# Kernel optimization log

Hardware: AMD Instinct MI355X
Metric: run time of the kernel (lower is better)

## Reference

```python
import jax, jax.numpy as jnp
import numpy as np

N_FEAT = 256
NUM_HEADS = 8
EPS = 1e-12  # torch F.normalize default eps


def setup_inputs() -> dict:
    key = jax.random.key(0)
    k1, k2, k3 = jax.random.split(key, 3)
    b, c, h, w = 1, N_FEAT, 64, 64
    x = jax.random.normal(k1, (b, c, h, w), dtype=jnp.float32)
    # 1x1 convs == channel GEMMs; store as (out_ch, in_ch) matrices
    w_qkv = jax.random.normal(k2, (3 * c, c), dtype=jnp.float32) * (1.0 / np.sqrt(c))
    w_proj = jax.random.normal(k3, (c, c), dtype=jnp.float32) * (1.0 / np.sqrt(c))
    temperature = jnp.ones((NUM_HEADS, 1, 1), dtype=jnp.float32)
    return {"x": x, "w_qkv": w_qkv, "w_proj": w_proj, "temperature": temperature}


def _l2norm(t):
    n = jnp.linalg.norm(t, axis=-1, keepdims=True)
    return t / jnp.maximum(n, EPS)


def reference(x, w_qkv, w_proj, temperature):
    b, c, h, w = x.shape
    heads = temperature.shape[0]
    d = c // heads
    hw = h * w
    xf = x.reshape(b, c, hw)
    # qkv 1x1 conv: (b, 3c, hw)
    qkv = jnp.einsum('oc,bcs->bos', w_qkv, xf)
    qkv = qkv.reshape(b, 3, heads, d, hw)
    q, k, v = qkv[:, 0], qkv[:, 1], qkv[:, 2]  # (b, heads, d, hw)
    q = jnp.swapaxes(q, -2, -1)  # (b, heads, hw, d)
    k = jnp.swapaxes(k, -2, -1)
    v = jnp.swapaxes(v, -2, -1)
    q = _l2norm(q)
    k = _l2norm(k)
    attn = jnp.einsum('bhsd,bhtd->bhst', q, k) * temperature[None]  # (b, heads, hw, hw)
    attn = jax.nn.softmax(attn, axis=-1)
    out = jnp.einsum('bhst,bhtd->bhsd', attn, v)  # (b, heads, hw, d)
    # faithful to torch: permute(0,2,1,3).reshape(b,c,h,w)
    out = out.transpose(0, 2, 1, 3).reshape(b, c, h, w)
    out = jnp.einsum('oc,bchw->bohw', w_proj, out)
    return out
```

## Files before the change

### kernel.cpp

```cpp
#include <hip/hip_runtime.h>
#include <stdint.h>

#define HW 4096
#define NH 8
#define NSPLIT 4
#define TSPLIT (HW / NSPLIT)

typedef __attribute__((ext_vector_type(8))) short short8;
typedef __attribute__((ext_vector_type(4))) float floatx4;

__device__ inline float bf2f(uint16_t u) {
  union { uint32_t i; float f; } v; v.i = ((uint32_t)u) << 16; return v.f;
}
__device__ inline float bflo(uint32_t u) {
  union { uint32_t i; float f; } v; v.i = u << 16; return v.f;
}
__device__ inline float bfhi(uint32_t u) {
  union { uint32_t i; float f; } v; v.i = u & 0xFFFF0000u; return v.f;
}
__device__ inline uint16_t f2bf(float f) {
  union { float f; uint32_t i; } v; v.f = f;
  uint32_t u = v.i; u += 0x7fffu + ((u >> 16) & 1u); return (uint16_t)(u >> 16);
}
__device__ inline uint32_t asu(float f) { union { float f; uint32_t i; } v; v.f = f; return v.i; }
__device__ inline uint32_t pk2r(float a, float b) {
#if __has_builtin(__builtin_amdgcn_cvt_pk_bf16_f32)
  union { short2 s; uint32_t u; } x;
  x.s = __builtin_amdgcn_cvt_pk_bf16_f32(a, b);
  return x.u;
#else
  return __builtin_amdgcn_perm(asu(b) + 0x8000u, asu(a) + 0x8000u, 0x07060302u);
#endif
}
__device__ inline short8 mk_s8(uint32_t a, uint32_t b, uint32_t c, uint32_t d) {
  union { uint32_t u[4]; short8 s; } x;
  x.u[0] = a; x.u[1] = b; x.u[2] = c; x.u[3] = d; return x.s;
}
__device__ inline bool is_f32(const uint32_t* Tp32) { return (Tp32[0] & 0xFFFFu) == 0u; }
__device__ inline float read_temp(const void* Tp, int h) {
  if (is_f32((const uint32_t*)Tp)) return ((const float*)Tp)[h];
  return bf2f(((const uint16_t*)Tp)[h]);
}

__global__ __launch_bounds__(256, 3) void k_gemm_qkv(const void* __restrict__ X,
                                                     const void* __restrict__ A,
                                                     const void* __restrict__ Tp,
                                                     uint16_t* __restrict__ Qr,
                                                     uint16_t* __restrict__ Kr,
                                                     uint16_t* __restrict__ Vr) {
  __shared__ uint16_t sA[2][128 * 64];
  __shared__ uint16_t sB[2][32 * 64];
  __shared__ uint16_t sXr[2][64 * 34];
  int tid = threadIdx.x;
  int w = tid >> 6, lane = tid & 63, lm = lane & 15, qd = lane >> 4;
  int n0 = blockIdx.x * 32, m0 = blockIdx.y * 128;
  bool aF32 = is_f32((const uint32_t*)Tp);
  floatx4 acc[2][2];
#pragma unroll
  for (int i = 0; i < 2; ++i)
#pragma unroll
    for (int j = 0; j < 2; ++j) acc[i][j] = (floatx4){0.f, 0.f, 0.f, 0.f};

  int cl = tid >> 2, sc = (tid & 3) * 8;
  int arow0 = tid >> 3, ac8 = tid & 7;

  float4 xfa, xfb; uint4 xua;
  float4 wfa[4][2]; uint4 wua[4];

#define QKV_LOADX(K0)                                                          \
  do {                                                                         \
    if (aF32) {                                                                \
      const float4* x4 = (const float4*)((const float*)X + ((K0) + cl) * HW + n0 + sc); \
      xfa = x4[0]; xfb = x4[1];                                                \
    } else {                                                                   \
      xua = *(const uint4*)((const uint16_t*)X + ((K0) + cl) * HW + n0 + sc);  \
    }                                                                          \
  } while (0)
#define QKV_LOADW(K0)                                                          \
  do {                                                                         \
    _Pragma("unroll") for (int r = 0; r < 4; ++r) {                            \
      int row = r * 32 + arow0;                                                \
      if (aF32) {                                                              \
        const float4* s4 = (const float4*)((const float*)A + (m0 + row) * 256 + (K0) + ac8 * 8); \
        wfa[r][0] = s4[0]; wfa[r][1] = s4[1];                                  \
      } else {                                                                 \
        wua[r] = *(const uint4*)((const uint16_t*)A + (m0 + row) * 256 + (K0) + ac8 * 8); \
      }                                                                        \
    }                                                                          \
  } while (0)

  QKV_LOADX(0);
  QKV_LOADW(0);
  int cur = 0;
  for (int ks = 0; ks < 4; ++ks) {
    int k0 = ks * 64;
    {
      uint32_t* l32 = (uint32_t*)sXr[cur];
      int base = cl * 17 + (sc >> 1);
      if (aF32) {
        l32[base + 0] = pk2r(xfa.x, xfa.y); l32[base + 1] = pk2r(xfa.z, xfa.w);
        l32[base + 2] = pk2r(xfb.x, xfb.y); l32[base + 3] = pk2r(xfb.z, xfb.w);
      } else {
        l32[base + 0] = xua.x; l32[base + 1] = xua.y;
        l32[base + 2] = xua.z; l32[base + 3] = xua.w;
      }
    }
#pragma unroll
    for (int r = 0; r < 4; ++r) {
      int row = r * 32 + arow0;
      uint4 v;
      if (aF32) {
        float4 a = wfa[r][0], b = wfa[r][1];
        v = make_uint4(pk2r(a.x, a.y), pk2r(a.z, a.w), pk2r(b.x, b.y), pk2r(b.z, b.w));
      } else {
        v = wua[r];
      }
      *(uint4*)(&sA[cur][row * 64 + (ac8 ^ (row & 7)) * 8]) = v;
    }
    if (ks < 3) {
      QKV_LOADX(k0 + 64);
      QKV_LOADW(k0 + 64);
    }
    __syncthreads();
    {
      int sl = tid >> 3, cs = (tid & 7) * 8;
      uint32_t wb[4];
#pragma unroll
      for (int j = 0; j < 4; ++j) {
        uint32_t lo = sXr[cur][(cs + 2 * j) * 34 + sl];
        uint32_t hi = sXr[cur][(cs + 2 * j + 1) * 34 + sl];
        wb[j] = lo | (hi << 16);
      }
      *(uint4*)(&sB[cur][sl * 64 + (((cs >> 3) ^ (sl & 7))) * 8]) =
          make_uint4(wb[0], wb[1], wb[2], wb[3]);
    }
    __syncthreads();
#pragma unroll
    for (int kk = 0; kk < 2; ++kk) {
      short8 af[2];
#pragma unroll
      for (int mt = 0; mt < 2; ++mt) {
        int row = w * 32 + mt * 16 + lm;
        af[mt] = *(const short8*)(&sA[cur][row * 64 + ((kk * 4 + qd) ^ (row & 7)) * 8]);
      }
#pragma unroll
      for (int nt = 0; nt < 2; ++nt) {
        int row = nt * 16 + lm;
        short8 bf = *(const short8*)(&sB[cur][row * 64 + ((kk * 4 + qd) ^ (row & 7)) * 8]);
#pragma unroll
        for (int mt = 0; mt < 2; ++mt)
          acc[mt][nt] = __builtin_amdgcn_mfma_f32_16x16x32_bf16(af[mt], bf, acc[mt][nt], 0, 0, 0);
      }
    }
    cur ^= 1;
  }
#undef QKV_LOADX
#undef QKV_LOADW
  int ow = m0 + w * 32;
  int type = ow >> 8;
  int hh = (ow >> 5) & 7;
  float tv = read_temp(Tp, hh);
#pragma unroll
  for (int nt = 0; nt < 2; ++nt) {
    int s = n0 + nt * 16 + lm;
    if (type < 2) {
      float ssq = 0.f;
#pragma unroll
      for (int mt = 0; mt < 2; ++mt)
#pragma unroll
        for (int r = 0; r < 4; ++r) ssq += acc[mt][nt][r] * acc[mt][nt][r];
      ssq += __shfl_xor(ssq, 16, 64);
      ssq += __shfl_xor(ssq, 32, 64);
      float sc2 = (type == 0 ? tv * 1.44269504088896340736f : 1.0f) /
                  fmaxf(sqrtf(ssq), 1e-12f);
      uint16_t* dst = (type == 0 ? Qr : Kr) + ((hh << 12) + s) * 32;
#pragma unroll
      for (int mt = 0; mt < 2; ++mt)
        *(uint2*)(dst + mt * 16 + qd * 4) =
            make_uint2(pk2r(acc[mt][nt][0] * sc2, acc[mt][nt][1] * sc2),
                       pk2r(acc[mt][nt][2] * sc2, acc[mt][nt][3] * sc2));
    } else {
#pragma unroll
      for (int mt = 0; mt < 2; ++mt)
#pragma unroll
        for (int r = 0; r < 4; ++r)
          Vr[(hh * 32 + mt * 16 + qd * 4 + r) * HW + s] = f2bf(acc[mt][nt][r]);
    }
  }
}

__global__ __launch_bounds__(256, 4) void k_attn(const uint16_t* __restrict__ Qr,
                                                 const uint16_t* __restrict__ Kr,
                                                 const uint16_t* __restrict__ Vr,
                                                 const void* __restrict__ Tp,
                                                 uint16_t* __restrict__ Op,
                                                 float* __restrict__ Lp) {
  __shared__ uint16_t sK[256 * 32];
  __shared__ uint16_t sV[32 * 256];
  int tid = threadIdx.x;
  int w = tid >> 6, lane = tid & 63, lm = lane & 15, qd = lane >> 4;
  int bid = blockIdx.x;
  int h = bid & 7;
  int j = bid >> 3;
  int sp = j & 3;
  int qb = j >> 2;
  int srow = qb * 128 + w * 32;
  const float c1 = 1.44269504088896340736f;
  float c2 = fabsf(read_temp(Tp, h)) * c1;
  short8 qf0 = *(const short8*)(Qr + ((h << 12) + srow + lm) * 32 + qd * 8);
  short8 qf1 = *(const short8*)(Qr + ((h << 12) + srow + 16 + lm) * 32 + qd * 8);
  const uint16_t* Kg = Kr + (h << 12) * 32;
  const uint16_t* Vg = Vr + (h * 32) * HW;
  floatx4 o00 = {0.f, 0.f, 0.f, 0.f}, o01 = {0.f, 0.f, 0.f, 0.f};
  floatx4 o10 = {0.f, 0.f, 0.f, 0.f}, o11 = {0.f, 0.f, 0.f, 0.f};
  floatx4 l0 = {0.f, 0.f, 0.f, 0.f}, l1 = {0.f, 0.f, 0.f, 0.f};
  const short8 ones8 = mk_s8(0x3F803F80u, 0x3F803F80u, 0x3F803F80u, 0x3F803F80u);
  const floatx4 zb = {-c2, -c2, -c2, -c2};
  const int kswz = (qd ^ ((lm >> 1) & 3)) * 8;

  int rK = tid >> 2, cK = tid & 3;
  uint16_t* dk0 = &sK[rK * 32 + (cK ^ ((rK >> 1) & 3)) * 8];
  const uint16_t* gk0 = Kg + (sp * TSPLIT + rK) * 32 + cK * 8;
  int dVb = tid >> 5, cVx = tid & 31;
  int s0x = dVb >> 1;
  bool sw = dVb & 1;
  uint16_t* dv0 = &sV[dVb * 256 + (cVx ^ s0x) * 8];
  uint16_t* dv1 = &sV[(dVb + 8) * 256 + (cVx ^ s0x ^ 4) * 8];
  const uint16_t* gv0 = Vg + dVb * HW + sp * TSPLIT + cVx * 8;

  uint4 rk0 = *(const uint4*)gk0;
  uint4 rk1 = *(const uint4*)(gk0 + 2048);
  uint4 rk2 = *(const uint4*)(gk0 + 4096);
  uint4 rk3 = *(const uint4*)(gk0 + 6144);
  uint4 rv0 = *(const uint4*)gv0;
  uint4 rv1 = *(const uint4*)(gv0 + 8 * HW);
  uint4 rv2 = *(const uint4*)(gv0 + 16 * HW);
  uint4 rv3 = *(const uint4*)(gv0 + 24 * HW);

  for (int i = 0; i < TSPLIT / 256; ++i) {
    __syncthreads();
    *(uint4*)dk0 = rk0;
    *(uint4*)(dk0 + 2048) = rk1;
    *(uint4*)(dk0 + 4096) = rk2;
    *(uint4*)(dk0 + 6144) = rk3;
    *(uint4*)dv0 = sw ? make_uint4(rv0.z, rv0.w, rv0.x, rv0.y) : rv0;
    *(uint4*)(dv0 + 4096) = sw ? make_uint4(rv2.z, rv2.w, rv2.x, rv2.y) : rv2;
    *(uint4*)dv1 = sw ? make_uint4(rv1.z, rv1.w, rv1.x, rv1.y) : rv1;
    *(uint4*)(dv1 + 4096) = sw ? make_uint4(rv3.z, rv3.w, rv3.x, rv3.y) : rv3;
    if (i + 1 < TSPLIT / 256) {
      gk0 += 256 * 32; gv0 += 256;
      rk0 = *(const uint4*)gk0;
      rk1 = *(const uint4*)(gk0 + 2048);
      rk2 = *(const uint4*)(gk0 + 4096);
      rk3 = *(const uint4*)(gk0 + 6144);
      rv0 = *(const uint4*)gv0;
      rv1 = *(const uint4*)(gv0 + 8 * HW);
      rv2 = *(const uint4*)(gv0 + 16 * HW);
      rv3 = *(const uint4*)(gv0 + 24 * HW);
    }
    asm volatile("s_waitcnt lgkmcnt(0)\n\ts_barrier" ::: "memory");
#pragma unroll
    for (int nt = 0; nt < 8; ++nt) {
      short8 kfa = *(const short8*)(&sK[(nt * 32 + lm) * 32 + kswz]);
      short8 kfb = *(const short8*)(&sK[(nt * 32 + 16 + lm) * 32 + kswz]);
      int gpa = (nt * 8 + qd) ^ lm;
      int gpb = (nt * 8 + 4 + qd) ^ lm;
      uint2 va0 = *(const uint2*)(&sV[lm * 256 + gpa * 4]);
      uint2 vb0 = *(const uint2*)(&sV[lm * 256 + gpb * 4]);
      uint2 va1 = *(const uint2*)(&sV[(lm + 16) * 256 + gpa * 4]);
      uint2 vb1 = *(const uint2*)(&sV[(lm + 16) * 256 + gpb * 4]);
      short8 vv0 = mk_s8(va0.x, va0.y, vb0.x, vb0.y);
      short8 vv1 = mk_s8(va1.x, va1.y, vb1.x, vb1.y);
      floatx4 sa = __builtin_amdgcn_mfma_f32_16x16x32_bf16(kfa, qf0, zb, 0, 0, 0);
      floatx4 sb = __builtin_amdgcn_mfma_f32_16x16x32_bf16(kfb, qf0, zb, 0, 0, 0);
      short8 pa = mk_s8(
          pk2r(__builtin_amdgcn_exp2f(sa[0]), __builtin_amdgcn_exp2f(sa[1])),
          pk2r(__builtin_amdgcn_exp2f(sa[2]), __builtin_amdgcn_exp2f(sa[3])),
          pk2r(__builtin_amdgcn_exp2f(sb[0]), __builtin_amdgcn_exp2f(sb[1])),
          pk2r(__builtin_amdgcn_exp2f(sb[2]), __builtin_amdgcn_exp2f(sb[3])));
      o00 = __builtin_amdgcn_mfma_f32_16x16x32_bf16(pa, vv0, o00, 0, 0, 0);
      o01 = __builtin_amdgcn_mfma_f32_16x16x32_bf16(pa, vv1, o01, 0, 0, 0);
      l0  = __builtin_amdgcn_mfma_f32_16x16x32_bf16(pa, ones8, l0, 0, 0, 0);
      sa = __builtin_amdgcn_mfma_f32_16x16x32_bf16(kfa, qf1, zb, 0, 0, 0);
      sb = __builtin_amdgcn_mfma_f32_16x16x32_bf16(kfb, qf1, zb, 0, 0, 0);
      pa = mk_s8(
          pk2r(__builtin_amdgcn_exp2f(sa[0]), __builtin_amdgcn_exp2f(sa[1])),
          pk2r(__builtin_amdgcn_exp2f(sa[2]), __builtin_amdgcn_exp2f(sa[3])),
          pk2r(__builtin_amdgcn_exp2f(sb[0]), __builtin_amdgcn_exp2f(sb[1])),
          pk2r(__builtin_amdgcn_exp2f(sb[2]), __builtin_amdgcn_exp2f(sb[3])));
      o10 = __builtin_amdgcn_mfma_f32_16x16x32_bf16(pa, vv0, o10, 0, 0, 0);
      o11 = __builtin_amdgcn_mfma_f32_16x16x32_bf16(pa, vv1, o11, 0, 0, 0);
      l1  = __builtin_amdgcn_mfma_f32_16x16x32_bf16(pa, ones8, l1, 0, 0, 0);
    }
  }
  int sb_ = (sp * NH + h) * HW + srow;
  uint16_t* op = Op + (size_t)sb_ * 32;
#pragma unroll
  for (int r = 0; r < 4; ++r) {
    op[(qd * 4 + r) * 32 + lm] = f2bf(o00[r]);
    op[(qd * 4 + r) * 32 + 16 + lm] = f2bf(o01[r]);
    op[(16 * 32) + (qd * 4 + r) * 32 + lm] = f2bf(o10[r]);
    op[(16 * 32) + (qd * 4 + r) * 32 + 16 + lm] = f2bf(o11[r]);
  }
  if (lm == 0) {
#pragma unroll
    for (int r = 0; r < 4; ++r) {
      Lp[sb_ + qd * 4 + r] = l0[r];
      Lp[sb_ + 16 + qd * 4 + r] = l1[r];
    }
  }
}

__global__ __launch_bounds__(256, 2) void k_gemm_proj(const void* __restrict__ A,
                                                      const uint16_t* __restrict__ Op,
                                                      const float* __restrict__ Lp,
                                                      void* __restrict__ C,
                                                      const uint32_t* __restrict__ Tp32) {
  __shared__ uint16_t sA[2][64 * 64];
  __shared__ uint16_t sB[2][32 * 64];
  __shared__ float sOp[2][64 * 33];
  int tid = threadIdx.x;
  int w = tid >> 6, lane = tid & 63, lm = lane & 15, qd = lane >> 4;
  int n0 = blockIdx.x * 32, m0 = blockIdx.y * 64;
  int h = (n0 >> 5) & 7, slo = n0 >> 8;
  bool aF32 = is_f32(Tp32);
  floatx4 acc[2];
  acc[0] = (floatx4){0.f, 0.f, 0.f, 0.f};
  acc[1] = (floatx4){0.f, 0.f, 0.f, 0.f};
  int cl = tid >> 2, dp = (tid & 3) * 8;
  int dd = tid >> 3, spart = (tid & 7) * 8;
  int arow0 = tid >> 3, ac8 = tid & 7;

  uint4 ga[NSPLIT]; float glp[NSPLIT];
  float4 wfa[2][2]; uint4 wua[2];

#define PRJ_LOADG(K0)                                                          \
  do {                                                                         \
    int s = slo + 16 * ((K0) + cl);                                            \
    _Pragma("unroll") for (int sp = 0; sp < NSPLIT; ++sp) {                    \
      size_t gj = (size_t)(sp * NH + h) * HW + s;                              \
      glp[sp] = Lp[gj];                                                        \
      ga[sp] = *(const uint4*)(Op + gj * 32 + dp);                             \
    }                                                                          \
  } while (0)
#define PRJ_LOADW(K0)                                                          \
  do {                                                                         \
    _Pragma("unroll") for (int r = 0; r < 2; ++r) {                            \
      int row = r * 32 + arow0;                                                \
      if (aF32) {                                                              \
        const float4* s4 = (const float4*)((const float*)A + (m0 + row) * 256 + (K0) + ac8 * 8); \
        wfa[r][0] = s4[0]; wfa[r][1] = s4[1];                                  \
      } else {                                                                 \
        wua[r] = *(const uint4*)((const uint16_t*)A + (m0 + row) * 256 + (K0) + ac8 * 8); \
      }                                                                        \
    }                                                                          \
  } while (0)

  PRJ_LOADG(0);
  PRJ_LOADW(0);
  int cur = 0;
  for (int k0 = 0; k0 < 256; k0 += 64) {
    {
      float L = 0.f;
      float a[8];
#pragma unroll
      for (int q = 0; q < 8; ++q) a[q] = 0.f;
#pragma unroll
      for (int sp = 0; sp < NSPLIT; ++sp) {
        L += glp[sp];
        uint4 x = ga[sp];
        a[0] += bflo(x.x); a[1] += bfhi(x.x); a[2] += bflo(x.y); a[3] += bfhi(x.y);
        a[4] += bflo(x.z); a[5] += bfhi(x.z); a[6] += bflo(x.w); a[7] += bfhi(x.w);
      }
      float inv = __builtin_amdgcn_rcpf(L);
#pragma unroll
      for (int q = 0; q < 8; ++q) sOp[cur][cl * 33 + dp + q] = a[q] * inv;
    }
#pragma unroll
    for (int r = 0; r < 2; ++r) {
      int row = r * 32 + arow0;
      uint4 v;
      if (aF32) {
        float4 a = wfa[r][0], b = wfa[r][1];
        v = make_uint4(pk2r(a.x, a.y), pk2r(a.z, a.w), pk2r(b.x, b.y), pk2r(b.z, b.w));
      } else {
        v = wua[r];
      }
      *(uint4*)(&sA[cur][row * 64 + (ac8 ^ (row & 7)) * 8]) = v;
    }
    if (k0 < 192) {
      PRJ_LOADG(k0 + 64);
      PRJ_LOADW(k0 + 64);
    }
    __syncthreads();
    {
      float b[8];
#pragma unroll
      for (int q = 0; q < 8; ++q) b[q] = sOp[cur][(spart + q) * 33 + dd];
      *(uint4*)(&sB[cur][dd * 64 + ((spart >> 3) ^ (dd & 7)) * 8]) =
          make_uint4(pk2r(b[0], b[1]), pk2r(b[2], b[3]),
                     pk2r(b[4], b[5]), pk2r(b[6], b[7]));
    }
    __syncthreads();
#pragma unroll
    for (int kk = 0; kk < 2; ++kk) {
      int arow = w * 16 + lm;
      short8 af = *(const short8*)(&sA[cur][arow * 64 + ((kk * 4 + qd) ^ (arow & 7)) * 8]);
#pragma unroll
      for (int nt = 0; nt < 2; ++nt) {
        int row = nt * 16 + lm;
        short8 bf = *(const short8*)(&sB[cur][row * 64 + ((kk * 4 + qd) ^ (row & 7)) * 8]);
        acc[nt] = __builtin_amdgcn_mfma_f32_16x16x32_bf16(af, bf, acc[nt], 0, 0, 0);
      }
    }
    cur ^= 1;
  }
#undef PRJ_LOADG
#undef PRJ_LOADW
  bool f32o = is_f32(Tp32);
#pragma unroll
  for (int nt = 0; nt < 2; ++nt)
#pragma unroll
    for (int r = 0; r < 4; ++r) {
      int row = m0 + w * 16 + qd * 4 + r;
      int col = n0 + nt * 16 + lm;
      if (f32o) ((float*)C)[row * HW + col] = acc[nt][r];
      else ((uint16_t*)C)[row * HW + col] = f2bf(acc[nt][r]);
    }
}

extern "C" void kernel_launch(void* const* d_in, const int* in_sizes, int n_in,
                              void* d_out, int out_size, void* d_ws, size_t ws_size,
                              hipStream_t stream) {
  const void* X  = d_in[0];
  const void* Wq = d_in[1];
  const void* Wp = d_in[2];
  const void* Tp = d_in[3];
  const uint32_t* Tp32 = (const uint32_t*)Tp;
  uint16_t* ws = (uint16_t*)d_ws;
  uint16_t* Qr = ws;
  uint16_t* Kr = Qr + NH * HW * 32;
  uint16_t* Vr = Kr + NH * HW * 32;
  uint16_t* Op = Vr + NH * 32 * HW;
  float* Lp = (float*)(Op + (size_t)NSPLIT * NH * HW * 32);

  k_gemm_qkv<<<dim3(128, 6), 256, 0, stream>>>(X, Wq, Tp, Qr, Kr, Vr);
  k_attn<<<dim3(1024), 256, 0, stream>>>(Qr, Kr, Vr, Tp, Op, Lp);
  k_gemm_proj<<<dim3(128, 4), 256, 0, stream>>>(Wp, Op, Lp, d_out, Tp32);
}
```

Baseline: 105.9 us.

## Load K fragments straight from global and double-buffer V in LDS

K tiles are no longer staged through shared memory. Each lane now reads its MFMA K fragments directly from global memory, prefetched two tiles ahead in registers. V moves to a double-buffered LDS array, so the next tile is written after compute and the leading __syncthreads before the stores goes away. The intent is to cut LDS traffic and one barrier per iteration. The cost is global-load latency sitting on the MFMA critical path, and K being re-read from L2 by every wave instead of shared within the block.

```diff
diff --git a/kernel.cpp b/kernel.cpp
--- a/kernel.cpp
+++ b/kernel.cpp
@@ -195,8 +195,7 @@
                                                  const void* __restrict__ Tp,
                                                  uint16_t* __restrict__ Op,
                                                  float* __restrict__ Lp) {
-  __shared__ uint16_t sK[256 * 32];
-  __shared__ uint16_t sV[32 * 256];
+  __shared__ uint16_t sV[2][32 * 256];
   int tid = threadIdx.x;
   int w = tid >> 6, lane = tid & 63, lm = lane & 15, qd = lane >> 4;
   int bid = blockIdx.x;
@@ -216,59 +215,59 @@
   floatx4 l0 = {0.f, 0.f, 0.f, 0.f}, l1 = {0.f, 0.f, 0.f, 0.f};
   const short8 ones8 = mk_s8(0x3F803F80u, 0x3F803F80u, 0x3F803F80u, 0x3F803F80u);
   const floatx4 zb = {-c2, -c2, -c2, -c2};
-  const int kswz = (qd ^ ((lm >> 1) & 3)) * 8;
-
-  int rK = tid >> 2, cK = tid & 3;
-  uint16_t* dk0 = &sK[rK * 32 + (cK ^ ((rK >> 1) & 3)) * 8];
-  const uint16_t* gk0 = Kg + (sp * TSPLIT + rK) * 32 + cK * 8;
+
+  const uint16_t* kp = Kg + (size_t)(sp * TSPLIT + lm) * 32 + qd * 8;
+
   int dVb = tid >> 5, cVx = tid & 31;
   int s0x = dVb >> 1;
   bool sw = dVb & 1;
-  uint16_t* dv0 = &sV[dVb * 256 + (cVx ^ s0x) * 8];
-  uint16_t* dv1 = &sV[(dVb + 8) * 256 + (cVx ^ s0x ^ 4) * 8];
+  int dv0o = dVb * 256 + (cVx ^ s0x) * 8;
+  int dv1o = (dVb + 8) * 256 + (cVx ^ s0x ^ 4) * 8;
   const uint16_t* gv0 = Vg + dVb * HW + sp * TSPLIT + cVx * 8;
 
-  uint4 rk0 = *(const uint4*)gk0;
-  uint4 rk1 = *(const uint4*)(gk0 + 2048);
-  uint4 rk2 = *(const uint4*)(gk0 + 4096);
-  uint4 rk3 = *(const uint4*)(gk0 + 6144);
   uint4 rv0 = *(const uint4*)gv0;
   uint4 rv1 = *(const uint4*)(gv0 + 8 * HW);
   uint4 rv2 = *(const uint4*)(gv0 + 16 * HW);
   uint4 rv3 = *(const uint4*)(gv0 + 24 * HW);
+  {
+    uint16_t* b = &sV[0][0];
+    *(uint4*)(b + dv0o) = sw ? make_uint4(rv0.z, rv0.w, rv0.x, rv0.y) : rv0;
+    *(uint4*)(b + dv0o + 4096) = sw ? make_uint4(rv2.z, rv2.w, rv2.x, rv2.y) : rv2;
+    *(uint4*)(b + dv1o) = sw ? make_uint4(rv1.z, rv1.w, rv1.x, rv1.y) : rv1;
+    *(uint4*)(b + dv1o + 4096) = sw ? make_uint4(rv3.z, rv3.w, rv3.x, rv3.y) : rv3;
+  }
+  {
+    gv0 += 256;
+    rv0 = *(const uint4*)gv0;
+    rv1 = *(const uint4*)(gv0 + 8 * HW);
+    rv2 = *(const uint4*)(gv0 + 16 * HW);
+    rv3 = *(const uint4*)(gv0 + 24 * HW);
+  }
 
   for (int i = 0; i < TSPLIT / 256; ++i) {
-    __syncthreads();
-    *(uint4*)dk0 = rk0;
-    *(uint4*)(dk0 + 2048) = rk1;
-    *(uint4*)(dk0 + 4096) = rk2;
-    *(uint4*)(dk0 + 6144) = rk3;
-    *(uint4*)dv0 = sw ? make_uint4(rv0.z, rv0.w, rv0.x, rv0.y) : rv0;
-    *(uint4*)(dv0 + 4096) = sw ? make_uint4(rv2.z, rv2.w, rv2.x, rv2.y) : rv2;
-    *(uint4*)dv1 = sw ? make_uint4(rv1.z, rv1.w, rv1.x, rv1.y) : rv1;
-    *(uint4*)(dv1 + 4096) = sw ? make_uint4(rv3.z, rv3.w, rv3.x, rv3.y) : rv3;
-    if (i + 1 < TSPLIT / 256) {
-      gk0 += 256 * 32; gv0 += 256;
-      rk0 = *(const uint4*)gk0;
-      rk1 = *(const uint4*)(gk0 + 2048);
-      rk2 = *(const uint4*)(gk0 + 4096);
-      rk3 = *(const uint4*)(gk0 + 6144);
-      rv0 = *(const uint4*)gv0;
-      rv1 = *(const uint4*)(gv0 + 8 * HW);
-      rv2 = *(const uint4*)(gv0 + 16 * HW);
-      rv3 = *(const uint4*)(gv0 + 24 * HW);
-    }
+    const uint16_t* kt = kp + i * 256 * 32;
+    short8 k0a = *(const short8*)kt;
+    short8 k0b = *(const short8*)(kt + 512);
+    short8 k1a = *(const short8*)(kt + 1024);
+    short8 k1b = *(const short8*)(kt + 1536);
     asm volatile("s_waitcnt lgkmcnt(0)\n\ts_barrier" ::: "memory");
+    const uint16_t* sVb = &sV[i & 1][0];
 #pragma unroll
     for (int nt = 0; nt < 8; ++nt) {
-      short8 kfa = *(const short8*)(&sK[(nt * 32 + lm) * 32 + kswz]);
-      short8 kfb = *(const short8*)(&sK[(nt * 32 + 16 + lm) * 32 + kswz]);
+      short8 kfa = k0a, kfb = k0b;
+      if (nt < 6) {
+        k0a = k1a; k0b = k1b;
+        k1a = *(const short8*)(kt + (nt + 2) * 1024);
+        k1b = *(const short8*)(kt + (nt + 2) * 1024 + 512);
+      } else if (nt == 6) {
+        k0a = k1a; k0b = k1b;
+      }
       int gpa = (nt * 8 + qd) ^ lm;
       int gpb = (nt * 8 + 4 + qd) ^ lm;
-      uint2 va0 = *(const uint2*)(&sV[lm * 256 + gpa * 4]);
-      uint2 vb0 = *(const uint2*)(&sV[lm * 256 + gpb * 4]);
-      uint2 va1 = *(const uint2*)(&sV[(lm + 16) * 256 + gpa * 4]);
-      uint2 vb1 = *(const uint2*)(&sV[(lm + 16) * 256 + gpb * 4]);
+      uint2 va0 = *(const uint2*)(sVb + lm * 256 + gpa * 4);
+      uint2 vb0 = *(const uint2*)(sVb + lm * 256 + gpb * 4);
+      uint2 va1 = *(const uint2*)(sVb + (lm + 16) * 256 + gpa * 4);
+      uint2 vb1 = *(const uint2*)(sVb + (lm + 16) * 256 + gpb * 4);
       short8 vv0 = mk_s8(va0.x, va0.y, vb0.x, vb0.y);
       short8 vv1 = mk_s8(va1.x, va1.y, vb1.x, vb1.y);
       floatx4 sa = __builtin_amdgcn_mfma_f32_16x16x32_bf16(kfa, qf0, zb, 0, 0, 0);
@@ -292,6 +291,20 @@
       o11 = __builtin_amdgcn_mfma_f32_16x16x32_bf16(pa, vv1, o11, 0, 0, 0);
       l1  = __builtin_amdgcn_mfma_f32_16x16x32_bf16(pa, ones8, l1, 0, 0, 0);
     }
+    if (i + 1 < TSPLIT / 256) {
+      uint16_t* b = &sV[(i + 1) & 1][0];
+      *(uint4*)(b + dv0o) = sw ? make_uint4(rv0.z, rv0.w, rv0.x, rv0.y) : rv0;
+      *(uint4*)(b + dv0o + 4096) = sw ? make_uint4(rv2.z, rv2.w, rv2.x, rv2.y) : rv2;
+      *(uint4*)(b + dv1o) = sw ? make_uint4(rv1.z, rv1.w, rv1.x, rv1.y) : rv1;
+      *(uint4*)(b + dv1o + 4096) = sw ? make_uint4(rv3.z, rv3.w, rv3.x, rv3.y) : rv3;
+      if (i + 2 < TSPLIT / 256) {
+        gv0 += 256;
+        rv0 = *(const uint4*)gv0;
+        rv1 = *(const uint4*)(gv0 + 8 * HW);
+        rv2 = *(const uint4*)(gv0 + 16 * HW);
+        rv3 = *(const uint4*)(gv0 + 24 * HW);
+      }
+    }
   }
   int sb_ = (sp * NH + h) * HW + srow;
   uint16_t* op = Op + (size_t)sb_ * 32;
```

After: 108.0 us. 2.0% more time.

## Software-pipeline QK^T MFMAs one tile ahead of exp and PV, stagger prefetches

Applied to the files above, without the earlier changes.

Restructures the attention inner loop so the QK^T score MFMAs for tile nt are issued one iteration ahead of the exp2/pack and PV MFMAs for tile nt-1, using double-buffered score registers. This lets the exp transcendental work overlap with independent MFMA work instead of waiting on fresh MFMA results. The global prefetches of the next V and K chunks are moved inside the inner loop at staggered points, and the outer loop is unrolled. It raises register pressure, which could hurt occupancy under the 3-wave launch bound.

```diff
diff --git a/kernel.cpp b/kernel.cpp
--- a/kernel.cpp
+++ b/kernel.cpp
@@ -35,6 +35,13 @@
 __device__ inline short8 mk_s8(uint32_t a, uint32_t b, uint32_t c, uint32_t d) {
   union { uint32_t u[4]; short8 s; } x;
   x.u[0] = a; x.u[1] = b; x.u[2] = c; x.u[3] = d; return x.s;
+}
+__device__ inline short8 pexp8(floatx4 a, floatx4 b) {
+  return mk_s8(
+      pk2r(__builtin_amdgcn_exp2f(a[0]), __builtin_amdgcn_exp2f(a[1])),
+      pk2r(__builtin_amdgcn_exp2f(a[2]), __builtin_amdgcn_exp2f(a[3])),
+      pk2r(__builtin_amdgcn_exp2f(b[0]), __builtin_amdgcn_exp2f(b[1])),
+      pk2r(__builtin_amdgcn_exp2f(b[2]), __builtin_amdgcn_exp2f(b[3])));
 }
 __device__ inline bool is_f32(const uint32_t* Tp32) { return (Tp32[0] & 0xFFFFu) == 0u; }
 __device__ inline float read_temp(const void* Tp, int h) {
@@ -237,7 +244,9 @@
   uint4 rv2 = *(const uint4*)(gv0 + 16 * HW);
   uint4 rv3 = *(const uint4*)(gv0 + 24 * HW);
 
+#pragma unroll
   for (int i = 0; i < TSPLIT / 256; ++i) {
+    const bool PREF = (i + 1 < TSPLIT / 256);
     __syncthreads();
     *(uint4*)dk0 = rk0;
     *(uint4*)(dk0 + 2048) = rk1;
@@ -247,50 +256,58 @@
     *(uint4*)(dv0 + 4096) = sw ? make_uint4(rv2.z, rv2.w, rv2.x, rv2.y) : rv2;
     *(uint4*)dv1 = sw ? make_uint4(rv1.z, rv1.w, rv1.x, rv1.y) : rv1;
     *(uint4*)(dv1 + 4096) = sw ? make_uint4(rv3.z, rv3.w, rv3.x, rv3.y) : rv3;
-    if (i + 1 < TSPLIT / 256) {
-      gk0 += 256 * 32; gv0 += 256;
-      rk0 = *(const uint4*)gk0;
-      rk1 = *(const uint4*)(gk0 + 2048);
-      rk2 = *(const uint4*)(gk0 + 4096);
-      rk3 = *(const uint4*)(gk0 + 6144);
-      rv0 = *(const uint4*)gv0;
-      rv1 = *(const uint4*)(gv0 + 8 * HW);
-      rv2 = *(const uint4*)(gv0 + 16 * HW);
-      rv3 = *(const uint4*)(gv0 + 24 * HW);
-    }
     asm volatile("s_waitcnt lgkmcnt(0)\n\ts_barrier" ::: "memory");
-#pragma unroll
-    for (int nt = 0; nt < 8; ++nt) {
-      short8 kfa = *(const short8*)(&sK[(nt * 32 + lm) * 32 + kswz]);
-      short8 kfb = *(const short8*)(&sK[(nt * 32 + 16 + lm) * 32 + kswz]);
-      int gpa = (nt * 8 + qd) ^ lm;
-      int gpb = (nt * 8 + 4 + qd) ^ lm;
+    floatx4 pa0s[2], pb0s[2], pa1s[2], pb1s[2];
+    {
+      short8 kfa = *(const short8*)(&sK[lm * 32 + kswz]);
+      short8 kfb = *(const short8*)(&sK[(16 + lm) * 32 + kswz]);
+      pa0s[0] = __builtin_amdgcn_mfma_f32_16x16x32_bf16(kfa, qf0, zb, 0, 0, 0);
+      pb0s[0] = __builtin_amdgcn_mfma_f32_16x16x32_bf16(kfb, qf0, zb, 0, 0, 0);
+      pa1s[0] = __builtin_amdgcn_mfma_f32_16x16x32_bf16(kfa, qf1, zb, 0, 0, 0);
+      pb1s[0] = __builtin_amdgcn_mfma_f32_16x16x32_bf16(kfb, qf1, zb, 0, 0, 0);
+    }
+#pragma unroll
+    for (int nt = 1; nt <= 8; ++nt) {
+      const int cu = (nt - 1) & 1, nx = nt & 1;
+      if (nt < 8) {
+        short8 kfa = *(const short8*)(&sK[(nt * 32 + lm) * 32 + kswz]);
+        short8 kfb = *(const short8*)(&sK[(nt * 32 + 16 + lm) * 32 + kswz]);
+        pa0s[nx] = __builtin_amdgcn_mfma_f32_16x16x32_bf16(kfa, qf0, zb, 0, 0, 0);
+        pb0s[nx] = __builtin_amdgcn_mfma_f32_16x16x32_bf16(kfb, qf0, zb, 0, 0, 0);
+        pa1s[nx] = __builtin_amdgcn_mfma_f32_16x16x32_bf16(kfa, qf1, zb, 0, 0, 0);
+        pb1s[nx] = __builtin_amdgcn_mfma_f32_16x16x32_bf16(kfb, qf1, zb, 0, 0, 0);
+      }
+      const int pm = nt - 1;
+      int gpa = (pm * 8 + qd) ^ lm;
+      int gpb = (pm * 8 + 4 + qd) ^ lm;
       uint2 va0 = *(const uint2*)(&sV[lm * 256 + gpa * 4]);
       uint2 vb0 = *(const uint2*)(&sV[lm * 256 + gpb * 4]);
       uint2 va1 = *(const uint2*)(&sV[(lm + 16) * 256 + gpa * 4]);
       uint2 vb1 = *(const uint2*)(&sV[(lm + 16) * 256 + gpb * 4]);
+      if (PREF && nt == 4) {
+        gv0 += 256;
+        rv0 = *(const uint4*)gv0;
+        rv1 = *(const uint4*)(gv0 + 8 * HW);
+        rv2 = *(const uint4*)(gv0 + 16 * HW);
+        rv3 = *(const uint4*)(gv0 + 24 * HW);
+      }
+      if (PREF && nt == 6) {
+        gk0 += 256 * 32;
+        rk0 = *(const uint4*)gk0;
+        rk1 = *(const uint4*)(gk0 + 2048);
+        rk2 = *(const uint4*)(gk0 + 4096);
+        rk3 = *(const uint4*)(gk0 + 6144);
+      }
+      short8 pa = pexp8(pa0s[cu], pb0s[cu]);
+      short8 pb = pexp8(pa1s[cu], pb1s[cu]);
       short8 vv0 = mk_s8(va0.x, va0.y, vb0.x, vb0.y);
       short8 vv1 = mk_s8(va1.x, va1.y, vb1.x, vb1.y);
-      floatx4 sa = __builtin_amdgcn_mfma_f32_16x16x32_bf16(kfa, qf0, zb, 0, 0, 0);
-      floatx4 sb = __builtin_amdgcn_mfma_f32_16x16x32_bf16(kfb, qf0, zb, 0, 0, 0);
-      short8 pa = mk_s8(
-          pk2r(__builtin_amdgcn_exp2f(sa[0]), __builtin_amdgcn_exp2f(sa[1])),
-          pk2r(__builtin_amdgcn_exp2f(sa[2]), __builtin_amdgcn_exp2f(sa[3])),
-          pk2r(__builtin_amdgcn_exp2f(sb[0]), __builtin_amdgcn_exp2f(sb[1])),
-          pk2r(__builtin_amdgcn_exp2f(sb[2]), __builtin_amdgcn_exp2f(sb[3])));
       o00 = __builtin_amdgcn_mfma_f32_16x16x32_bf16(pa, vv0, o00, 0, 0, 0);
+      o10 = __builtin_amdgcn_mfma_f32_16x16x32_bf16(pb, vv0, o10, 0, 0, 0);
       o01 = __builtin_amdgcn_mfma_f32_16x16x32_bf16(pa, vv1, o01, 0, 0, 0);
+      o11 = __builtin_amdgcn_mfma_f32_16x16x32_bf16(pb, vv1, o11, 0, 0, 0);
       l0  = __builtin_amdgcn_mfma_f32_16x16x32_bf16(pa, ones8, l0, 0, 0, 0);
-      sa = __builtin_amdgcn_mfma_f32_16x16x32_bf16(kfa, qf1, zb, 0, 0, 0);
-      sb = __builtin_amdgcn_mfma_f32_16x16x32_bf16(kfb, qf1, zb, 0, 0, 0);
-      pa = mk_s8(
-          pk2r(__builtin_amdgcn_exp2f(sa[0]), __builtin_amdgcn_exp2f(sa[1])),
-          pk2r(__builtin_amdgcn_exp2f(sa[2]), __builtin_amdgcn_exp2f(sa[3])),
-          pk2r(__builtin_amdgcn_exp2f(sb[0]), __builtin_amdgcn_exp2f(sb[1])),
-          pk2r(__builtin_amdgcn_exp2f(sb[2]), __builtin_amdgcn_exp2f(sb[3])));
-      o10 = __builtin_amdgcn_mfma_f32_16x16x32_bf16(pa, vv0, o10, 0, 0, 0);
-      o11 = __builtin_amdgcn_mfma_f32_16x16x32_bf16(pa, vv1, o11, 0, 0, 0);
-      l1  = __builtin_amdgcn_mfma_f32_16x16x32_bf16(pa, ones8, l1, 0, 0, 0);
+      l1  = __builtin_amdgcn_mfma_f32_16x16x32_bf16(pb, ones8, l1, 0, 0, 0);
     }
   }
   int sb_ = (sp * NH + h) * HW + srow;
```

Result: no change. 106.3 us (+0.4%).
